# Kernel optimization log

Measured on AMD Instinct MI355X. Metric: run time of the kernel, lower is better.

The kernel has to match this reference:

```python
import jax, jax.numpy as jnp
import numpy as np


def _make_grid(h, w):
    """Replicates gen_grid_coordinates_optimized(h, w, stride=1) vectorized in numpy.
    Returns (h*3, w*3, 2) float32 grid in grid_sample convention (x=col, y=row, in [-1,1])."""
    pi = np.pi
    dphi = pi / h
    dtheta = 2 * pi / w
    tp, tt, icp = np.tan(dphi), np.tan(dtheta), 1.0 / np.cos(dphi)
    xys = np.array([[(-tt, icp * tp), (0, tp), (tt, icp * tp)],
                    [(-tt, 0), (1, 1), (tt, 0)],
                    [(-tt, -icp * tp), (0, -tp), (tt, -icp * tp)]], dtype=np.float64)
    xk, yk = xys[..., 0], xys[..., 1]          # (3,3) kernel offsets on tangent plane
    rho = np.sqrt(xk ** 2 + yk ** 2)
    v = np.arctan(rho)
    cv, sv = np.cos(v), np.sin(v)
    rr = np.arange(h, dtype=np.float64)
    cc = np.arange(w, dtype=np.float64)
    phi = -((rr + 0.5) / h * pi - pi / 2)      # (h,)
    theta = (cc + 0.5) / w * 2 * pi - pi       # (w,)
    cph = np.cos(phi)[:, None, None]
    sph = np.sin(phi)[:, None, None]
    # (h,3,3) ; clip guards fp roundoff at poles (mathematically |arg|<=1)
    new_phi = np.arcsin(np.clip(cv * sph + yk * sv * cph / rho, -1.0, 1.0))
    dtheta_off = np.arctan(xk * sv / (rho * cph * cv - yk * sph * sv))  # (h,3,3)
    new_theta = theta[None, :, None, None] + dtheta_off[:, None]        # (h,w,3,3)
    new_r = np.broadcast_to(((-new_phi + pi / 2) * h / pi - 0.5)[:, None], (h, w, 3, 3)).copy()
    new_c = (new_theta + pi) * w / (2 * pi) - 0.5
    new_c = (new_c + w) % w
    # kernel center samples the pixel itself
    new_r[:, :, 1, 1] = rr[:, None]
    new_c[:, :, 1, 1] = cc[None, :]
    gy = new_r * 2 / h - 1
    gx = new_c * 2 / w - 1
    grid = np.stack([gx, gy], axis=-1)                      # (h,w,ki,kj,2)
    grid = grid.transpose(0, 2, 1, 3, 4).reshape(h * 3, w * 3, 2)
    return grid.astype(np.float32)


def _grid_sample_bilinear(x, grid):
    """F.grid_sample(mode='bilinear', align_corners=True, padding_mode='zeros').
    x: (N,C,H,W), grid: (Hg,Wg,2) shared across batch. Returns (N,C,Hg,Wg)."""
    N, C, H, W = x.shape
    ix = (grid[..., 0] + 1) * 0.5 * (W - 1)
    iy = (grid[..., 1] + 1) * 0.5 * (H - 1)
    x0 = jnp.floor(ix)
    y0 = jnp.floor(iy)
    x1, y1 = x0 + 1, y0 + 1
    xflat = x.reshape(N, C, H * W)

    def corner(yc, xc, wgt):
        valid = (xc >= 0) & (xc <= W - 1) & (yc >= 0) & (yc <= H - 1)
        xi = jnp.clip(xc, 0, W - 1).astype(jnp.int32)
        yi = jnp.clip(yc, 0, H - 1).astype(jnp.int32)
        idx = (yi * W + xi).reshape(-1)
        v = xflat[:, :, idx].reshape(N, C, *xc.shape)
        return v * (wgt * valid)[None, None]

    out = (corner(y0, x0, (x1 - ix) * (y1 - iy))
           + corner(y0, x1, (ix - x0) * (y1 - iy))
           + corner(y1, x0, (x1 - ix) * (iy - y0))
           + corner(y1, x1, (ix - x0) * (iy - y0)))
    return out


def setup_inputs() -> dict:
    key = jax.random.key(0)
    k1, k2 = jax.random.split(key)
    B, Cin, Cout, H, W = 4, 16, 32, 256, 512
    x = jax.random.normal(k1, (B, Cin, H, W), dtype=jnp.float32)
    fan_out = Cout * 9  # kaiming_normal fan_out, relu gain
    weight = jax.random.normal(k2, (Cout, Cin, 3, 3), dtype=jnp.float32) * np.sqrt(2.0 / fan_out)
    bias = jnp.zeros((Cout,), dtype=jnp.float32)
    grid = jnp.asarray(_make_grid(H, W))  # (H*3, W*3, 2) constant spherical warp
    return {"x": x, "weight": weight, "bias": bias, "grid": grid}


def reference(x, weight, bias, grid):
    s = _grid_sample_bilinear(x, grid)  # (N,C,3H,3W)
    out = jax.lax.conv_general_dilated(
        s, weight, window_strides=(3, 3), padding='VALID',
        dimension_numbers=('NCHW', 'OIHW', 'NCHW'))
    return out + bias[None, :, None, None]
```

## Files before the change

kernel.cpp:

```cpp
#include <hip/hip_runtime.h>

#define HH 256
#define WW 512
#define NCIN 16
#define NCOUT 32
#define NB 4
#define KP 168
#define WKP 168
#define NPIX 128

typedef _Float16 h2 __attribute__((ext_vector_type(2)));
typedef _Float16 half4 __attribute__((ext_vector_type(4)));
typedef _Float16 half8 __attribute__((ext_vector_type(8)));
typedef float f32x4 __attribute__((ext_vector_type(4)));

#define XT_OFF   0u
#define XTAB_OFF 16777216u
#define WTAB_OFF (16777216u + 9437184u)
#define YTAB_OFF (16777216u + 9437184u + 16384u)
#define WS_NEED  (YTAB_OFF + 36864u)

__global__ __launch_bounds__(256) void precompute_all(const float* __restrict__ x,
                                                      const float* __restrict__ w,
                                                      const float* __restrict__ grid,
                                                      _Float16* __restrict__ xh,
                                                      float2* __restrict__ xtab,
                                                      _Float16* __restrict__ wtab,
                                                      float4* __restrict__ ytab) {
    const float2* g2 = reinterpret_cast<const float2*>(grid);
    if (blockIdx.x < 2048) {
        const int lb = (blockIdx.x & 7) * 256 + (blockIdx.x >> 3);
        const int t = lb * 256 + threadIdx.x;
        const int c = t & (WW - 1);
        const int r = (t >> 9) & (HH - 1);
        const int b = t >> 17;
        const float* xp = x + ((size_t)(b * NCIN) * HH + r) * WW + c;
        half8 h0, h1;
#pragma unroll
        for (int ci = 0; ci < 8; ++ci)  h0[ci] = (_Float16)xp[(size_t)ci * (HH * WW)];
#pragma unroll
        for (int ci = 0; ci < 8; ++ci)  h1[ci] = (_Float16)xp[(size_t)(8 + ci) * (HH * WW)];
        half8* op = reinterpret_cast<half8*>(xh) + (size_t)t * 2;
        op[0] = h0;
        op[1] = h1;
        return;
    }
    if (blockIdx.x < 2048 + 4608) {
        const int t = (blockIdx.x - 2048) * 256 + threadIdx.x;
        const int c = t & (WW - 1);
        const int u = t >> 9;
        const int r = u / 9, tap = u - r * 9;
        const int kr = tap / 3, kc = tap - kr * 3;
        const float gx = g2[(size_t)(r * 3 + kr) * (WW * 3) + (c * 3 + kc)].x;
        const float ix = ((gx + 1.0f) * 0.5f) * (float)(WW - 1);
        const float x0f = floorf(ix);
        xtab[t] = make_float2(ix - x0f, __int_as_float((int)x0f));
        return;
    }
    const int t = (blockIdx.x - 6656) * 256 + threadIdx.x;
    if (t < NCOUT * WKP) {
        const int co = t / WKP, kk = t - co * WKP;
        float v = 0.0f;
        if (kk < 144) v = w[co * 144 + (kk & 15) * 9 + (kk >> 4)];
        wtab[t] = (_Float16)v;
    } else if (t < NCOUT * WKP + HH * 9) {
        const int u = t - NCOUT * WKP;
        const int r = u / 9, tap = u - r * 9;
        const int kr = tap / 3, kc = tap - kr * 3;
        const float gy = g2[(size_t)(r * 3 + kr) * (WW * 3) + kc].y;
        const float iy = ((gy + 1.0f) * 0.5f) * (float)(HH - 1);
        const float y0f = floorf(iy);
        const float fy = iy - y0f;
        const int y0 = (int)y0f, y1 = y0 + 1;
        float wy0 = 1.0f - fy, wy1 = fy;
        if (y0 < 0 || y0 > HH - 1) wy0 = 0.0f;
        if (y1 < 0 || y1 > HH - 1) wy1 = 0.0f;
        const int cy0 = min(max(y0, 0), HH - 1), cy1 = min(max(y1, 0), HH - 1);
        ytab[u] = make_float4(wy0, wy1, __int_as_float(cy0), __int_as_float(cy1));
    }
}

__global__ __launch_bounds__(256, 3) void sphere_mfma_kernel(const _Float16* __restrict__ xh,
                                                             const float2* __restrict__ xtab,
                                                             const _Float16* __restrict__ wtab,
                                                             const float4* __restrict__ ytab,
                                                             const float* __restrict__ bias,
                                                             float* __restrict__ out) {
    __shared__ _Float16 Sl[NPIX * KP];
    const int tid = threadIdx.x, lane = tid & 63, wv = tid >> 6;
    const int col = lane & 15, g4 = lane >> 4;
    const int pxl = lane >> 1, h = lane & 1;
    const int px = wv * 32 + pxl;

    const int lb = ((blockIdx.x & 7) << 9) + (blockIdx.x >> 3);
    const int pixbase = lb << 7;
    const int b    = pixbase >> 17;
    const int rimg = (pixbase >> 9) & (HH - 1);
    const int c0   = pixbase & (WW - 1);

    {
        half8 z = {0, 0, 0, 0, 0, 0, 0, 0};
        *reinterpret_cast<half8*>(&Sl[px * KP + 144 + h * 8]) = z;
    }

    float wy0s[9], wy1s[9];
    int Rb0[9], Rb1[9];
#pragma unroll
    for (int t = 0; t < 9; ++t) {
        const float4 y = ytab[rimg * 9 + t];
        wy0s[t] = y.x;
        wy1s[t] = y.y;
        Rb0[t] = (b * HH + __float_as_int(y.z)) << 10;
        Rb1[t] = (b * HH + __float_as_int(y.w)) << 10;
    }

    const float2* xrow = xtab + (size_t)rimg * 9 * WW + (c0 + px);
    float2 f2s[9];
#pragma unroll
    for (int t = 0; t < 9; ++t) f2s[t] = xrow[t * WW];

    const half8* x8 = reinterpret_cast<const half8*>(xh);
    half8 A00[9], A01[9], A10[9], A11[9];
#pragma unroll
    for (int t = 0; t < 9; ++t) {
        const int x0 = __float_as_int(f2s[t].y);
        const int pb0 = Rb0[t] + (x0 << 1) + h;
        const int pb1 = Rb1[t] + (x0 << 1) + h;
        A00[t] = x8[pb0];
        A01[t] = x8[pb0 + 2];
        A10[t] = x8[pb1];
        A11[t] = x8[pb1 + 2];
    }

#pragma unroll
    for (int t = 0; t < 9; ++t) {
        const float fx = f2s[t].x;
        const float wx0 = 1.0f - fx;
        const float w00 = wx0 * wy0s[t], w01 = fx * wy0s[t];
        const float w10 = wx0 * wy1s[t], w11 = fx * wy1s[t];
        const _Float16 W00 = (_Float16)w00, W01 = (_Float16)w01;
        const _Float16 W10 = (_Float16)w10, W11 = (_Float16)w11;
        const half8 B00 = {W00, W00, W00, W00, W00, W00, W00, W00};
        const half8 B01 = {W01, W01, W01, W01, W01, W01, W01, W01};
        const half8 B10 = {W10, W10, W10, W10, W10, W10, W10, W10};
        const half8 B11 = {W11, W11, W11, W11, W11, W11, W11, W11};
        half8 pk = A00[t] * B00;
        pk += A01[t] * B01;
        pk += A10[t] * B10;
        pk += A11[t] * B11;
        *reinterpret_cast<half8*>(&Sl[px * KP + t * 16 + h * 8]) = pk;
    }

    half8 wA[5][2];
#pragma unroll
    for (int s = 0; s < 5; ++s)
#pragma unroll
        for (int m = 0; m < 2; ++m)
            wA[s][m] = *reinterpret_cast<const half8*>(wtab + (m * 16 + col) * WKP + s * 32 + g4 * 8);


    f32x4 acc[2][2] = {{{0.f, 0.f, 0.f, 0.f}, {0.f, 0.f, 0.f, 0.f}},
                       {{0.f, 0.f, 0.f, 0.f}, {0.f, 0.f, 0.f, 0.f}}};
#pragma unroll
    for (int s = 0; s < 5; ++s)
#pragma unroll
        for (int m = 0; m < 2; ++m) {
            const half8 bf = *reinterpret_cast<const half8*>(
                &Sl[(wv * 32 + m * 16 + col) * KP + s * 32 + g4 * 8]);
            acc[m][0] = __builtin_amdgcn_mfma_f32_16x16x32_f16(wA[s][0], bf, acc[m][0], 0, 0, 0);
            acc[m][1] = __builtin_amdgcn_mfma_f32_16x16x32_f16(wA[s][1], bf, acc[m][1], 0, 0, 0);
        }

#pragma unroll
    for (int m = 0; m < 2; ++m) {
        const int pix = c0 + wv * 32 + m * 16 + col;
        float* ob = out + (((size_t)(b * NCOUT) * HH + rimg) * WW) + pix;
#pragma unroll
        for (int mm = 0; mm < 2; ++mm)
#pragma unroll
            for (int r = 0; r < 4; ++r) {
                const int co = mm * 16 + g4 * 4 + r;
                ob[(size_t)co * (HH * WW)] = acc[m][mm][r] + bias[co];
            }
    }
}

__global__ __launch_bounds__(256) void sphere_conv_fallback(const float* __restrict__ x,
                                                            const float* __restrict__ weight,
                                                            const float* __restrict__ bias,
                                                            const float* __restrict__ grid,
                                                            float* __restrict__ out) {
    __shared__ float wlds[NCIN * 9 * NCOUT];
    const int tid = threadIdx.x;
    for (int e = tid; e < NCIN * 9 * NCOUT; e += 256) {
        const int co  = e & (NCOUT - 1);
        const int cik = e >> 5;
        wlds[e] = weight[co * (NCIN * 9) + cik];
    }
    __syncthreads();

    const int pindex = blockIdx.x * 256 + tid;
    const int c = pindex & (WW - 1);
    const int r = (pindex >> 9) & (HH - 1);
    const int b = pindex >> 17;

    float acc[NCOUT];
#pragma unroll
    for (int o = 0; o < NCOUT; ++o) acc[o] = 0.0f;

    const float2* g2 = reinterpret_cast<const float2*>(grid);

#pragma unroll 1
    for (int k = 0; k < 9; ++k) {
        const int kr = k / 3, kc = k - kr * 3;
        const float2 g = g2[(r * 3 + kr) * (WW * 3) + (c * 3 + kc)];
        const float ix = ((g.x + 1.0f) * 0.5f) * (float)(WW - 1);
        const float iy = ((g.y + 1.0f) * 0.5f) * (float)(HH - 1);
        const float x0f = floorf(ix), y0f = floorf(iy);
        const float fx = ix - x0f, fy = iy - y0f;
        const int x0 = (int)x0f, y0 = (int)y0f;
        const int x1 = x0 + 1, y1 = y0 + 1;
        float wx0 = 1.0f - fx, wx1 = fx, wy0 = 1.0f - fy, wy1 = fy;
        if (x0 < 0 || x0 > WW - 1) wx0 = 0.0f;
        if (x1 < 0 || x1 > WW - 1) wx1 = 0.0f;
        if (y0 < 0 || y0 > HH - 1) wy0 = 0.0f;
        if (y1 < 0 || y1 > HH - 1) wy1 = 0.0f;
        const int cx0 = min(max(x0, 0), WW - 1), cx1 = min(max(x1, 0), WW - 1);
        const int cy0 = min(max(y0, 0), HH - 1), cy1 = min(max(y1, 0), HH - 1);
        const float w00 = wx0 * wy0, w01 = wx1 * wy0, w10 = wx0 * wy1, w11 = wx1 * wy1;

#pragma unroll 1
        for (int ci = 0; ci < NCIN; ++ci) {
            const float* xb = x + (size_t)((b * NCIN + ci) * HH) * WW;
            const float a00 = xb[cy0 * WW + cx0];
            const float a01 = xb[cy0 * WW + cx1];
            const float a10 = xb[cy1 * WW + cx0];
            const float a11 = xb[cy1 * WW + cx1];
            const float s = w00 * a00 + w01 * a01 + w10 * a10 + w11 * a11;
            const float4* wl = reinterpret_cast<const float4*>(&wlds[(ci * 9 + k) * NCOUT]);
#pragma unroll
            for (int o = 0; o < 8; ++o) {
                const float4 wv = wl[o];
                acc[o * 4 + 0] += wv.x * s;
                acc[o * 4 + 1] += wv.y * s;
                acc[o * 4 + 2] += wv.z * s;
                acc[o * 4 + 3] += wv.w * s;
            }
        }
    }

    const int obase = ((b * NCOUT) * HH + r) * WW + c;
#pragma unroll
    for (int o = 0; o < NCOUT; ++o) {
        out[obase + o * (HH * WW)] = acc[o] + bias[o];
    }
}

extern "C" void kernel_launch(void* const* d_in, const int* in_sizes, int n_in,
                              void* d_out, int out_size, void* d_ws, size_t ws_size,
                              hipStream_t stream) {
    const float* x    = (const float*)d_in[0];
    const float* w    = (const float*)d_in[1];
    const float* bias = (const float*)d_in[2];
    const float* grid = (const float*)d_in[3];
    float* out = (float*)d_out;

    if (ws_size >= WS_NEED) {
        char* ws = (char*)d_ws;
        _Float16* xh   = (_Float16*)(ws + XT_OFF);
        float2*   xtab = (float2*)(ws + XTAB_OFF);
        _Float16* wtab = (_Float16*)(ws + WTAB_OFF);
        float4*   ytab = (float4*)(ws + YTAB_OFF);

        precompute_all<<<6686, 256, 0, stream>>>(x, w, grid, xh, xtab, wtab, ytab);
        sphere_mfma_kernel<<<4096, 256, 0, stream>>>(xh, xtab, wtab, ytab, bias, out);
    } else {
        sphere_conv_fallback<<<2048, 256, 0, stream>>>(x, w, bias, grid, out);
    }
}
```

Before: 56.43 us.

## Switch to 32x32x16 MFMA with K=144, shrink LDS row pad

Replaces the 16x16x32 MFMA tiling, which pads K to 160 and needs 20 MFMAs per wave, with nine 32x32x16 MFMAs that cover exactly K=144 (16 channels by 9 taps). This removes the zero-padding of the shared tile and cuts register use for the weight fragments. The LDS row stride drops from 168 to 152 halves, and launch bounds are raised to 4 blocks per SIMD to increase occupancy. The output store mapping changes to match the 32x32 accumulator layout, and LDS bank conflicts may differ with the new stride.

Measured after the change: 55.58 us. Within noise of the previous version (-1.5%).

```diff
diff --git a/kernel.cpp b/kernel.cpp
--- a/kernel.cpp
+++ b/kernel.cpp
@@ -5,14 +5,14 @@
 #define NCIN 16
 #define NCOUT 32
 #define NB 4
-#define KP 168
+#define KP 152
 #define WKP 168
 #define NPIX 128
 
-typedef _Float16 h2 __attribute__((ext_vector_type(2)));
 typedef _Float16 half4 __attribute__((ext_vector_type(4)));
 typedef _Float16 half8 __attribute__((ext_vector_type(8)));
 typedef float f32x4 __attribute__((ext_vector_type(4)));
+typedef float f32x16 __attribute__((ext_vector_type(16)));
 
 #define XT_OFF   0u
 #define XTAB_OFF 16777216u
@@ -80,7 +80,7 @@
     }
 }
 
-__global__ __launch_bounds__(256, 3) void sphere_mfma_kernel(const _Float16* __restrict__ xh,
+__global__ __launch_bounds__(256, 4) void sphere_mfma_kernel(const _Float16* __restrict__ xh,
                                                              const float2* __restrict__ xtab,
                                                              const _Float16* __restrict__ wtab,
                                                              const float4* __restrict__ ytab,
@@ -88,7 +88,7 @@
                                                              float* __restrict__ out) {
     __shared__ _Float16 Sl[NPIX * KP];
     const int tid = threadIdx.x, lane = tid & 63, wv = tid >> 6;
-    const int col = lane & 15, g4 = lane >> 4;
+    const int c32 = lane & 31, hi = lane >> 5;
     const int pxl = lane >> 1, h = lane & 1;
     const int px = wv * 32 + pxl;
 
@@ -97,11 +97,6 @@
     const int b    = pixbase >> 17;
     const int rimg = (pixbase >> 9) & (HH - 1);
     const int c0   = pixbase & (WW - 1);
-
-    {
-        half8 z = {0, 0, 0, 0, 0, 0, 0, 0};
-        *reinterpret_cast<half8*>(&Sl[px * KP + 144 + h * 8]) = z;
-    }
 
     float wy0s[9], wy1s[9];
     int Rb0[9], Rb1[9];
@@ -151,37 +146,26 @@
         *reinterpret_cast<half8*>(&Sl[px * KP + t * 16 + h * 8]) = pk;
     }
 
-    half8 wA[5][2];
-#pragma unroll
-    for (int s = 0; s < 5; ++s)
-#pragma unroll
-        for (int m = 0; m < 2; ++m)
-            wA[s][m] = *reinterpret_cast<const half8*>(wtab + (m * 16 + col) * WKP + s * 32 + g4 * 8);
-
-
-    f32x4 acc[2][2] = {{{0.f, 0.f, 0.f, 0.f}, {0.f, 0.f, 0.f, 0.f}},
-                       {{0.f, 0.f, 0.f, 0.f}, {0.f, 0.f, 0.f, 0.f}}};
-#pragma unroll
-    for (int s = 0; s < 5; ++s)
-#pragma unroll
-        for (int m = 0; m < 2; ++m) {
-            const half8 bf = *reinterpret_cast<const half8*>(
-                &Sl[(wv * 32 + m * 16 + col) * KP + s * 32 + g4 * 8]);
-            acc[m][0] = __builtin_amdgcn_mfma_f32_16x16x32_f16(wA[s][0], bf, acc[m][0], 0, 0, 0);
-            acc[m][1] = __builtin_amdgcn_mfma_f32_16x16x32_f16(wA[s][1], bf, acc[m][1], 0, 0, 0);
-        }
-
-#pragma unroll
-    for (int m = 0; m < 2; ++m) {
-        const int pix = c0 + wv * 32 + m * 16 + col;
-        float* ob = out + (((size_t)(b * NCOUT) * HH + rimg) * WW) + pix;
-#pragma unroll
-        for (int mm = 0; mm < 2; ++mm)
-#pragma unroll
-            for (int r = 0; r < 4; ++r) {
-                const int co = mm * 16 + g4 * 4 + r;
-                ob[(size_t)co * (HH * WW)] = acc[m][mm][r] + bias[co];
-            }
+    half8 wA[9];
+#pragma unroll
+    for (int t = 0; t < 9; ++t)
+        wA[t] = *reinterpret_cast<const half8*>(wtab + c32 * WKP + t * 16 + hi * 8);
+
+
+    f32x16 acc = {};
+#pragma unroll
+    for (int t = 0; t < 9; ++t) {
+        const half8 bf = *reinterpret_cast<const half8*>(
+            &Sl[(wv * 32 + c32) * KP + t * 16 + hi * 8]);
+        acc = __builtin_amdgcn_mfma_f32_32x32x16_f16(wA[t], bf, acc, 0, 0, 0);
+    }
+
+    const int pix = c0 + wv * 32 + c32;
+    float* ob = out + (((size_t)(b * NCOUT) * HH + rimg) * WW) + pix;
+#pragma unroll
+    for (int reg = 0; reg < 16; ++reg) {
+        const int co = (reg & 3) + 8 * (reg >> 2) + 4 * hi;
+        ob[(size_t)co * (HH * WW)] = acc[reg] + bias[co];
     }
 }
 
```
